# Optimization experiments

Measured on AMD Instinct MI355X. Metric: run time of the kernel, lower is better.

## Reference

```python
import jax, jax.numpy as jnp
import numpy as np

B, D, T = 16, 512, 2048
K, C = 8, 1024          # num_codebooks, codebook_size
CH = D // K             # chunk_size = 64
COMMIT = 0.25
EPS = 1e-8


def setup_inputs() -> dict:
    key = jax.random.key(0)
    k1, k2 = jax.random.split(key)
    x = jax.random.normal(k1, (B, D, T), dtype=jnp.float32)
    # kaiming-uniform-ish init for codebooks [K, C, CH]
    bound = float(np.sqrt(6.0 / CH))
    codebooks = jax.random.uniform(k2, (K, C, CH), dtype=jnp.float32,
                                   minval=-bound, maxval=bound)
    return {"x": x, "codebooks": codebooks}


def reference(x, codebooks):
    b, d, t = x.shape
    xc = x.reshape(b, K, CH, t)                       # [B,K,CH,T]
    x_norm = jnp.sum(xc * xc, axis=2)[:, :, None, :]  # [B,K,1,T]
    c_norm = jnp.sum(codebooks * codebooks, axis=2)[None, :, :, None]  # [1,K,C,1]
    cross = -2.0 * jnp.einsum('bkdt,kcd->bkct', xc, codebooks)         # [B,K,C,T]
    distances = x_norm + c_norm + cross
    indices = jnp.argmin(distances, axis=2)           # [B,K,T] int
    # gather nearest codewords -> [B,K,T,CH] -> [B,K,CH,T]
    q = codebooks[jnp.arange(K)[None, :, None], indices]
    q = jnp.transpose(q, (0, 1, 3, 2))                # [B,K,CH,T]
    # per-codebook usage histogram
    kk = jnp.broadcast_to(jnp.arange(K)[None, :, None], indices.shape)
    counts = jnp.zeros((K, C), dtype=jnp.float32).at[kk.ravel(), indices.ravel()].add(1.0)
    avg_probs = counts / (b * t)
    perplexity = jnp.exp(jnp.sum(-avg_probs * jnp.log(avg_probs + EPS), axis=1))
    # commitment losses
    sg = jax.lax.stop_gradient
    codebook_loss = jnp.mean((sg(xc) - q) ** 2)
    encoder_loss = jnp.mean((xc - sg(q)) ** 2)
    commit_loss = codebook_loss + COMMIT * encoder_loss
    # straight-through estimator
    quantized = xc + sg(q - xc)
    return quantized.reshape(b, d, t), commit_loss, perplexity
```

## Files before the change

kernel.cpp:

```cpp
#include <hip/hip_runtime.h>
#include <hip/hip_bf16.h>
#include <math.h>

#define B_   16
#define D_   512
#define T_   2048
#define K_   8
#define C_   1024
#define CH_  64
#define NEL_ (B_ * D_ * T_)
#define QOFF 16777216

#define WS_HCN   0
#define WS_CNT   32768
#define WS_SSE   65536
#define WS_CBS   66048

typedef __attribute__((ext_vector_type(8))) short   short8;
typedef __attribute__((ext_vector_type(8))) __bf16  bf16x8;
typedef __attribute__((ext_vector_type(4))) float   f32x4;

__device__ __forceinline__ unsigned short f2bf_rne(float f) {
    unsigned u = __builtin_bit_cast(unsigned, f);
    u = u + 0x7FFFu + ((u >> 16) & 1u);
    return (unsigned short)(u >> 16);
}

__device__ __forceinline__ void gload_lds16(const void* gsrc, void* ldst) {
    __builtin_amdgcn_global_load_lds(
        (const __attribute__((address_space(1))) unsigned int*)gsrc,
        (__attribute__((address_space(3))) unsigned int*)ldst,
        16, 0, 0);
}

__global__ void vq_prep(const float* __restrict__ cb,
                        unsigned char* __restrict__ cbS,
                        float* __restrict__ hcn) {
    int g   = blockIdx.x * 256 + threadIdx.x;
    int row = g >> 3;
    int s8  = g & 7;
    const float* src = cb + (size_t)row * CH_;

    short8 val;
#pragma unroll
    for (int j = 0; j < 8; ++j)
        val[j] = (short)f2bf_rne(-src[s8 * 8 + j]);
    *(short8*)(cbS + (size_t)row * 128 + ((s8 ^ (row & 7)) * 16)) = val;

    if (s8 == 0) {
        float s = 0.f;
#pragma unroll 8
        for (int ch = 0; ch < CH_; ++ch) {
            float v = src[ch];
            s = fmaf(v, v, s);
        }
        hcn[row] = 0.5f * s;
    }
}

#define LDSBUF 16384

__global__ __launch_bounds__(256, 4) void vq_main(
    const float* __restrict__ x,
    const float* __restrict__ cb,
    const unsigned char* __restrict__ cbS,
    const float* __restrict__ hcn,
    float* __restrict__ out,
    int* __restrict__ counts,
    double* __restrict__ sse)
{
    __shared__ __align__(16) unsigned char lds[2 * LDSBUF + 4096];
    float* hcnS = (float*)(lds + 2 * LDSBUF);

    const int tid  = threadIdx.x;
    const int lane = tid & 63;
    const int wave = tid >> 6;
    const int ln   = lane & 15;
    const int q    = lane >> 4;
    const int q4   = q * 4;

    const int bid = blockIdx.x;
    const int tc  = bid & 7;
    const int k   = (bid >> 3) & 7;
    const int b   = bid >> 6;
    const int t0  = tc * 256 + wave * 64;

    short8 bh[4][2];
    float  xn[4];
#pragma unroll
    for (int tt = 0; tt < 4; ++tt) {
        int t = t0 + tt * 16 + ln;
        float pn = 0.f;
#pragma unroll
        for (int ks = 0; ks < 2; ++ks) {
            const float* xp = x + ((size_t)(b * D_ + k * CH_ + ks * 32 + q * 8)) * T_ + t;
            short8 sh;
#pragma unroll
            for (int j = 0; j < 8; ++j) {
                float v = xp[(size_t)j * T_];
                pn = fmaf(v, v, pn);
                sh[j] = (short)f2bf_rne(v);
            }
            bh[tt][ks] = sh;
        }
        pn += __shfl_xor(pn, 16);
        pn += __shfl_xor(pn, 32);
        xn[tt] = pn;
    }

    const unsigned char* cbS_k = cbS + (size_t)k * C_ * 128;
    const float*         hcn_k = hcn + k * C_;

    for (int i = tid; i < C_; i += 256) hcnS[i] = hcn_k[i];

    {
        const unsigned char* src = cbS_k + wave * 4096 + lane * 16;
        unsigned char* dst = lds + wave * 4096;
#pragma unroll
        for (int i = 0; i < 4; ++i)
            gload_lds16(src + i * 1024, dst + i * 1024);
    }

    float md[4][4];
    int   mj[4][4];
#pragma unroll
    for (int tt = 0; tt < 4; ++tt)
#pragma unroll
        for (int r = 0; r < 4; ++r) { md[tt][r] = INFINITY; mj[tt][r] = 0; }

    for (int chunk = 0; chunk < 8; ++chunk) {
        __syncthreads();

        if (chunk < 7) {
            const unsigned char* src =
                cbS_k + (size_t)(chunk + 1) * 16384 + wave * 4096 + lane * 16;
            unsigned char* dst = lds + ((chunk + 1) & 1) * LDSBUF + wave * 4096;
#pragma unroll
            for (int i = 0; i < 4; ++i)
                gload_lds16(src + i * 1024, dst + i * 1024);
        }

        const unsigned char* buf = lds + (chunk & 1) * LDSBUF;
#pragma unroll
        for (int sub = 0; sub < 8; ++sub) {
            const unsigned char* rowb = buf + (sub * 16 + ln) * 128;
            f32x4 h4 = *(const f32x4*)(hcnS + chunk * 128 + sub * 16 + q4);
            f32x4 a[4];
#pragma unroll
            for (int tt = 0; tt < 4; ++tt) a[tt] = h4;
#pragma unroll
            for (int ks = 0; ks < 2; ++ks) {
                int cidx = ((ks * 4 + q) ^ (ln & 7)) * 16;
                bf16x8 ah = __builtin_bit_cast(bf16x8, *(const short8*)(rowb + cidx));
#pragma unroll
                for (int tt = 0; tt < 4; ++tt)
                    a[tt] = __builtin_amdgcn_mfma_f32_16x16x32_bf16(
                        ah, __builtin_bit_cast(bf16x8, bh[tt][ks]), a[tt], 0, 0, 0);
            }
            const int j = chunk * 8 + sub;
#pragma unroll
            for (int tt = 0; tt < 4; ++tt) {
#pragma unroll
                for (int r = 0; r < 4; ++r) {
                    bool lt = a[tt][r] < md[tt][r];
                    md[tt][r] = lt ? a[tt][r] : md[tt][r];
                    mj[tt][r] = lt ? j : mj[tt][r];
                }
            }
        }
    }

    double waveSse = 0.0;
    const float* cb_k = cb + (size_t)k * C_ * CH_;

#pragma unroll
    for (int tt = 0; tt < 4; ++tt) {
        const int t = t0 + tt * 16 + ln;

        float d1 = md[tt][0];
        int   c1 = mj[tt][0] * 16 + q4;
#pragma unroll
        for (int r = 1; r < 4; ++r) {
            float v  = md[tt][r];
            int   cv = mj[tt][r] * 16 + q4 + r;
            bool w = (v < d1) || (v == d1 && cv < c1);
            d1 = w ? v : d1;
            c1 = w ? cv : c1;
        }
#pragma unroll
        for (int off = 16; off <= 32; off <<= 1) {
            float ov = __shfl_xor(d1, off);
            int   oc = __shfl_xor(c1, off);
            bool w = (ov < d1) || (ov == d1 && oc < c1);
            d1 = w ? ov : d1;
            c1 = w ? oc : c1;
        }
        const int idx = c1;

        if (q == 0) {
            waveSse += (double)(xn[tt] + 2.0f * d1);
            atomicAdd(&counts[k * C_ + idx], 1);
        }

        const float* qrow = cb_k + (size_t)idx * CH_ + q * 16;
        float* op = out + ((size_t)(b * D_ + k * CH_ + q * 16)) * T_ + t;
#pragma unroll
        for (int jj = 0; jj < 4; ++jj) {
            float4 qv = *(const float4*)(qrow + 4 * jj);
            op[(size_t)(4 * jj + 0) * T_] = qv.x;
            op[(size_t)(4 * jj + 1) * T_] = qv.y;
            op[(size_t)(4 * jj + 2) * T_] = qv.z;
            op[(size_t)(4 * jj + 3) * T_] = qv.w;
        }
    }

    for (int off = 32; off > 0; off >>= 1) waveSse += __shfl_down(waveSse, off);
    if (lane == 0) atomicAdd(sse, waveSse);
}

__global__ void vq_final(const int* __restrict__ counts,
                         const double* __restrict__ sse,
                         float* __restrict__ out) {
    __shared__ double part[4];
    const int tid = threadIdx.x;
    const int k   = blockIdx.x;
    double local = 0.0;
    for (int j = tid; j < C_; j += 256) {
        double p = (double)counts[k * C_ + j] * (1.0 / (double)(B_ * T_));
        local += -p * log(p + 1e-8);
    }
    for (int off = 32; off > 0; off >>= 1) local += __shfl_down(local, off);
    if ((tid & 63) == 0) part[tid >> 6] = local;
    __syncthreads();
    if (tid == 0) {
        double sum = part[0] + part[1] + part[2] + part[3];
        out[QOFF + 1 + k] = (float)exp(sum);
        if (k == 0)
            out[QOFF] = (float)(1.25 * (*sse) / (double)NEL_);
    }
}

extern "C" void kernel_launch(void* const* d_in, const int* in_sizes, int n_in,
                              void* d_out, int out_size, void* d_ws, size_t ws_size,
                              hipStream_t stream) {
    const float* x  = (const float*)d_in[0];
    const float* cb = (const float*)d_in[1];
    float* out = (float*)d_out;

    float*         hcn    = (float*)((char*)d_ws + WS_HCN);
    int*           counts = (int*)((char*)d_ws + WS_CNT);
    double*        sse    = (double*)((char*)d_ws + WS_SSE);
    unsigned char* cbS    = (unsigned char*)((char*)d_ws + WS_CBS);

    hipMemsetAsync((char*)d_ws + WS_CNT, 0, 33024, stream);

    vq_prep<<<(K_ * C_ * 8) / 256, 256, 0, stream>>>(cb, cbS, hcn);
    vq_main<<<B_ * K_ * (T_ / 256), 256, 0, stream>>>(x, cb, cbS, hcn,
                                                      out, counts, sse);
    vq_final<<<K_, 256, 0, stream>>>(counts, sse, out);
}
```

Measured before the change: 222.3 us.

## Use 512-thread blocks, stage indices in LDS for coalesced output, fold memset into prep

Doubles the block size to 8 waves, each handling 32 time steps instead of 64, which halves per-wave MFMA accumulators and raises occupancy. Winning indices are staged in LDS so the output writeback becomes float4 stores contiguous along T instead of scattered scalar stores. The counters and SSE are zeroed inside the prep kernel, removing the separate memset launch. The trade-off is that each codebook tile read from LDS is reused across fewer time columns, and an extra block-wide barrier is added before writeback.

```diff
diff --git a/kernel.cpp b/kernel.cpp
--- a/kernel.cpp
+++ b/kernel.cpp
@@ -19,6 +19,7 @@
 typedef __attribute__((ext_vector_type(8))) short   short8;
 typedef __attribute__((ext_vector_type(8))) __bf16  bf16x8;
 typedef __attribute__((ext_vector_type(4))) float   f32x4;
+typedef __attribute__((ext_vector_type(4))) int     i32x4;
 
 __device__ __forceinline__ unsigned short f2bf_rne(float f) {
     unsigned u = __builtin_bit_cast(unsigned, f);
@@ -35,8 +36,13 @@
 
 __global__ void vq_prep(const float* __restrict__ cb,
                         unsigned char* __restrict__ cbS,
-                        float* __restrict__ hcn) {
+                        float* __restrict__ hcn,
+                        int* __restrict__ counts,
+                        double* __restrict__ sse) {
     int g   = blockIdx.x * 256 + threadIdx.x;
+    if (g < K_ * C_) counts[g] = 0;
+    if (g == 0) *sse = 0.0;
+
     int row = g >> 3;
     int s8  = g & 7;
     const float* src = cb + (size_t)row * CH_;
@@ -60,7 +66,7 @@
 
 #define LDSBUF 16384
 
-__global__ __launch_bounds__(256, 4) void vq_main(
+__global__ __launch_bounds__(512, 8) void vq_main(
     const float* __restrict__ x,
     const float* __restrict__ cb,
     const unsigned char* __restrict__ cbS,
@@ -69,8 +75,9 @@
     int* __restrict__ counts,
     double* __restrict__ sse)
 {
-    __shared__ __align__(16) unsigned char lds[2 * LDSBUF + 4096];
+    __shared__ __align__(16) unsigned char lds[2 * LDSBUF + 4096 + 1024];
     float* hcnS = (float*)(lds + 2 * LDSBUF);
+    int*   idxS = (int*)(lds + 2 * LDSBUF + 4096);
 
     const int tid  = threadIdx.x;
     const int lane = tid & 63;
@@ -83,13 +90,14 @@
     const int tc  = bid & 7;
     const int k   = (bid >> 3) & 7;
     const int b   = bid >> 6;
-    const int t0  = tc * 256 + wave * 64;
-
-    short8 bh[4][2];
-    float  xn[4];
-#pragma unroll
-    for (int tt = 0; tt < 4; ++tt) {
-        int t = t0 + tt * 16 + ln;
+    const int t0  = tc * 256;
+    const int tw  = t0 + wave * 32;
+
+    short8 bh[2][2];
+    float  xn[2];
+#pragma unroll
+    for (int tt = 0; tt < 2; ++tt) {
+        int t = tw + tt * 16 + ln;
         float pn = 0.f;
 #pragma unroll
         for (int ks = 0; ks < 2; ++ks) {
@@ -111,20 +119,20 @@
     const unsigned char* cbS_k = cbS + (size_t)k * C_ * 128;
     const float*         hcn_k = hcn + k * C_;
 
-    for (int i = tid; i < C_; i += 256) hcnS[i] = hcn_k[i];
+    for (int i = tid; i < C_; i += 512) hcnS[i] = hcn_k[i];
 
     {
-        const unsigned char* src = cbS_k + wave * 4096 + lane * 16;
-        unsigned char* dst = lds + wave * 4096;
-#pragma unroll
-        for (int i = 0; i < 4; ++i)
+        const unsigned char* src = cbS_k + wave * 2048 + lane * 16;
+        unsigned char* dst = lds + wave * 2048;
+#pragma unroll
+        for (int i = 0; i < 2; ++i)
             gload_lds16(src + i * 1024, dst + i * 1024);
     }
 
-    float md[4][4];
-    int   mj[4][4];
-#pragma unroll
-    for (int tt = 0; tt < 4; ++tt)
+    float md[2][4];
+    int   mj[2][4];
+#pragma unroll
+    for (int tt = 0; tt < 2; ++tt)
 #pragma unroll
         for (int r = 0; r < 4; ++r) { md[tt][r] = INFINITY; mj[tt][r] = 0; }
 
@@ -133,10 +141,10 @@
 
         if (chunk < 7) {
             const unsigned char* src =
-                cbS_k + (size_t)(chunk + 1) * 16384 + wave * 4096 + lane * 16;
-            unsigned char* dst = lds + ((chunk + 1) & 1) * LDSBUF + wave * 4096;
-#pragma unroll
-            for (int i = 0; i < 4; ++i)
+                cbS_k + (size_t)(chunk + 1) * 16384 + wave * 2048 + lane * 16;
+            unsigned char* dst = lds + ((chunk + 1) & 1) * LDSBUF + wave * 2048;
+#pragma unroll
+            for (int i = 0; i < 2; ++i)
                 gload_lds16(src + i * 1024, dst + i * 1024);
         }
 
@@ -145,21 +153,21 @@
         for (int sub = 0; sub < 8; ++sub) {
             const unsigned char* rowb = buf + (sub * 16 + ln) * 128;
             f32x4 h4 = *(const f32x4*)(hcnS + chunk * 128 + sub * 16 + q4);
-            f32x4 a[4];
-#pragma unroll
-            for (int tt = 0; tt < 4; ++tt) a[tt] = h4;
+            f32x4 a[2];
+            a[0] = h4;
+            a[1] = h4;
 #pragma unroll
             for (int ks = 0; ks < 2; ++ks) {
                 int cidx = ((ks * 4 + q) ^ (ln & 7)) * 16;
                 bf16x8 ah = __builtin_bit_cast(bf16x8, *(const short8*)(rowb + cidx));
 #pragma unroll
-                for (int tt = 0; tt < 4; ++tt)
+                for (int tt = 0; tt < 2; ++tt)
                     a[tt] = __builtin_amdgcn_mfma_f32_16x16x32_bf16(
                         ah, __builtin_bit_cast(bf16x8, bh[tt][ks]), a[tt], 0, 0, 0);
             }
             const int j = chunk * 8 + sub;
 #pragma unroll
-            for (int tt = 0; tt < 4; ++tt) {
+            for (int tt = 0; tt < 2; ++tt) {
 #pragma unroll
                 for (int r = 0; r < 4; ++r) {
                     bool lt = a[tt][r] < md[tt][r];
@@ -171,12 +179,9 @@
     }
 
     double waveSse = 0.0;
-    const float* cb_k = cb + (size_t)k * C_ * CH_;
-
-#pragma unroll
-    for (int tt = 0; tt < 4; ++tt) {
-        const int t = t0 + tt * 16 + ln;
-
+
+#pragma unroll
+    for (int tt = 0; tt < 2; ++tt) {
         float d1 = md[tt][0];
         int   c1 = mj[tt][0] * 16 + q4;
 #pragma unroll
@@ -195,27 +200,40 @@
             d1 = w ? ov : d1;
             c1 = w ? oc : c1;
         }
-        const int idx = c1;
 
         if (q == 0) {
             waveSse += (double)(xn[tt] + 2.0f * d1);
-            atomicAdd(&counts[k * C_ + idx], 1);
-        }
-
-        const float* qrow = cb_k + (size_t)idx * CH_ + q * 16;
-        float* op = out + ((size_t)(b * D_ + k * CH_ + q * 16)) * T_ + t;
-#pragma unroll
-        for (int jj = 0; jj < 4; ++jj) {
-            float4 qv = *(const float4*)(qrow + 4 * jj);
-            op[(size_t)(4 * jj + 0) * T_] = qv.x;
-            op[(size_t)(4 * jj + 1) * T_] = qv.y;
-            op[(size_t)(4 * jj + 2) * T_] = qv.z;
-            op[(size_t)(4 * jj + 3) * T_] = qv.w;
+            atomicAdd(&counts[k * C_ + c1], 1);
+            idxS[wave * 32 + tt * 16 + ln] = c1;
         }
     }
 
     for (int off = 32; off > 0; off >>= 1) waveSse += __shfl_down(waveSse, off);
     if (lane == 0) atomicAdd(sse, waveSse);
+
+    __syncthreads();
+
+    const float* cb_k = cb + (size_t)k * C_ * CH_;
+    i32x4 idx4 = *(const i32x4*)(idxS + 4 * lane);
+
+    float vals[4][8];
+#pragma unroll
+    for (int m = 0; m < 4; ++m) {
+        const float* rp = cb_k + (size_t)idx4[m] * CH_ + wave * 8;
+        f32x4 a0 = *(const f32x4*)rp;
+        f32x4 a1 = *(const f32x4*)(rp + 4);
+#pragma unroll
+        for (int jj = 0; jj < 4; ++jj) {
+            vals[m][jj]     = a0[jj];
+            vals[m][jj + 4] = a1[jj];
+        }
+    }
+#pragma unroll
+    for (int rr = 0; rr < 8; ++rr) {
+        f32x4 v = { vals[0][rr], vals[1][rr], vals[2][rr], vals[3][rr] };
+        *(f32x4*)(out + ((size_t)(b * D_ + k * CH_ + wave * 8 + rr)) * T_
+                      + t0 + 4 * lane) = v;
+    }
 }
 
 __global__ void vq_final(const int* __restrict__ counts,
@@ -252,10 +270,8 @@
     double*        sse    = (double*)((char*)d_ws + WS_SSE);
     unsigned char* cbS    = (unsigned char*)((char*)d_ws + WS_CBS);
 
-    hipMemsetAsync((char*)d_ws + WS_CNT, 0, 33024, stream);
-
-    vq_prep<<<(K_ * C_ * 8) / 256, 256, 0, stream>>>(cb, cbS, hcn);
-    vq_main<<<B_ * K_ * (T_ / 256), 256, 0, stream>>>(x, cb, cbS, hcn,
+    vq_prep<<<(K_ * C_ * 8) / 256, 256, 0, stream>>>(cb, cbS, hcn, counts, sse);
+    vq_main<<<B_ * K_ * (T_ / 256), 512, 0, stream>>>(x, cb, cbS, hcn,
                                                       out, counts, sse);
     vq_final<<<K_, 256, 0, stream>>>(counts, sse, out);
 }
```

New measurement: 247.4 us. 11.3% more time.

## Stage argmin indices in LDS and write output with coalesced float4 stores

Applied to the files above, without the earlier changes.

The output gather is restructured so each block stages its chosen codeword indices in shared memory, then each thread writes four consecutive time steps per channel as a float4 store instead of scattered scalar stores strided by T. Argmin slot indices are packed into one 32-bit register per tile to cut register pressure. The separate memset is folded into the prep kernel, and launch bounds drop from 4 to 2 waves per SIMD hint. Costs are an extra block barrier and a small LDS buffer, and the looser launch bounds may change occupancy.

```diff
diff --git a/kernel.cpp b/kernel.cpp
--- a/kernel.cpp
+++ b/kernel.cpp
@@ -19,6 +19,7 @@
 typedef __attribute__((ext_vector_type(8))) short   short8;
 typedef __attribute__((ext_vector_type(8))) __bf16  bf16x8;
 typedef __attribute__((ext_vector_type(4))) float   f32x4;
+typedef __attribute__((ext_vector_type(4))) int     i32x4;
 
 __device__ __forceinline__ unsigned short f2bf_rne(float f) {
     unsigned u = __builtin_bit_cast(unsigned, f);
@@ -35,8 +36,13 @@
 
 __global__ void vq_prep(const float* __restrict__ cb,
                         unsigned char* __restrict__ cbS,
-                        float* __restrict__ hcn) {
+                        float* __restrict__ hcn,
+                        int* __restrict__ counts,
+                        double* __restrict__ sse) {
     int g   = blockIdx.x * 256 + threadIdx.x;
+    if (g < K_ * C_) counts[g] = 0;
+    if (g == 0) *sse = 0.0;
+
     int row = g >> 3;
     int s8  = g & 7;
     const float* src = cb + (size_t)row * CH_;
@@ -60,7 +66,7 @@
 
 #define LDSBUF 16384
 
-__global__ __launch_bounds__(256, 4) void vq_main(
+__global__ __launch_bounds__(256, 2) void vq_main(
     const float* __restrict__ x,
     const float* __restrict__ cb,
     const unsigned char* __restrict__ cbS,
@@ -69,8 +75,9 @@
     int* __restrict__ counts,
     double* __restrict__ sse)
 {
-    __shared__ __align__(16) unsigned char lds[2 * LDSBUF + 4096];
+    __shared__ __align__(16) unsigned char lds[2 * LDSBUF + 4096 + 1024];
     float* hcnS = (float*)(lds + 2 * LDSBUF);
+    int*   idxS = (int*)(lds + 2 * LDSBUF + 4096);
 
     const int tid  = threadIdx.x;
     const int lane = tid & 63;
@@ -83,13 +90,14 @@
     const int tc  = bid & 7;
     const int k   = (bid >> 3) & 7;
     const int b   = bid >> 6;
-    const int t0  = tc * 256 + wave * 64;
+    const int t0b = tc * 256;
+    const int tw  = t0b + wave * 64;
 
     short8 bh[4][2];
     float  xn[4];
 #pragma unroll
     for (int tt = 0; tt < 4; ++tt) {
-        int t = t0 + tt * 16 + ln;
+        int t = tw + tt * 16 + ln;
         float pn = 0.f;
 #pragma unroll
         for (int ks = 0; ks < 2; ++ks) {
@@ -121,12 +129,14 @@
             gload_lds16(src + i * 1024, dst + i * 1024);
     }
 
-    float md[4][4];
-    int   mj[4][4];
-#pragma unroll
-    for (int tt = 0; tt < 4; ++tt)
-#pragma unroll
-        for (int r = 0; r < 4; ++r) { md[tt][r] = INFINITY; mj[tt][r] = 0; }
+    float    md[4][4];
+    unsigned mjp[4];
+#pragma unroll
+    for (int tt = 0; tt < 4; ++tt) {
+        mjp[tt] = 0u;
+#pragma unroll
+        for (int r = 0; r < 4; ++r) md[tt][r] = INFINITY;
+    }
 
     for (int chunk = 0; chunk < 8; ++chunk) {
         __syncthreads();
@@ -157,32 +167,30 @@
                     a[tt] = __builtin_amdgcn_mfma_f32_16x16x32_bf16(
                         ah, __builtin_bit_cast(bf16x8, bh[tt][ks]), a[tt], 0, 0, 0);
             }
-            const int j = chunk * 8 + sub;
+            const unsigned j = (unsigned)(chunk * 8 + sub);
 #pragma unroll
             for (int tt = 0; tt < 4; ++tt) {
 #pragma unroll
                 for (int r = 0; r < 4; ++r) {
                     bool lt = a[tt][r] < md[tt][r];
                     md[tt][r] = lt ? a[tt][r] : md[tt][r];
-                    mj[tt][r] = lt ? j : mj[tt][r];
+                    unsigned upd = (mjp[tt] & ~(0xFFu << (8 * r))) | (j << (8 * r));
+                    mjp[tt] = lt ? upd : mjp[tt];
                 }
             }
         }
     }
 
     double waveSse = 0.0;
-    const float* cb_k = cb + (size_t)k * C_ * CH_;
 
 #pragma unroll
     for (int tt = 0; tt < 4; ++tt) {
-        const int t = t0 + tt * 16 + ln;
-
         float d1 = md[tt][0];
-        int   c1 = mj[tt][0] * 16 + q4;
+        int   c1 = (int)(mjp[tt] & 0xFFu) * 16 + q4;
 #pragma unroll
         for (int r = 1; r < 4; ++r) {
             float v  = md[tt][r];
-            int   cv = mj[tt][r] * 16 + q4 + r;
+            int   cv = (int)((mjp[tt] >> (8 * r)) & 0xFFu) * 16 + q4 + r;
             bool w = (v < d1) || (v == d1 && cv < c1);
             d1 = w ? v : d1;
             c1 = w ? cv : c1;
@@ -195,27 +203,35 @@
             d1 = w ? ov : d1;
             c1 = w ? oc : c1;
         }
-        const int idx = c1;
 
         if (q == 0) {
             waveSse += (double)(xn[tt] + 2.0f * d1);
-            atomicAdd(&counts[k * C_ + idx], 1);
-        }
-
-        const float* qrow = cb_k + (size_t)idx * CH_ + q * 16;
-        float* op = out + ((size_t)(b * D_ + k * CH_ + q * 16)) * T_ + t;
-#pragma unroll
-        for (int jj = 0; jj < 4; ++jj) {
-            float4 qv = *(const float4*)(qrow + 4 * jj);
-            op[(size_t)(4 * jj + 0) * T_] = qv.x;
-            op[(size_t)(4 * jj + 1) * T_] = qv.y;
-            op[(size_t)(4 * jj + 2) * T_] = qv.z;
-            op[(size_t)(4 * jj + 3) * T_] = qv.w;
+            atomicAdd(&counts[k * C_ + c1], 1);
+            idxS[wave * 64 + tt * 16 + ln] = c1;
         }
     }
 
     for (int off = 32; off > 0; off >>= 1) waveSse += __shfl_down(waveSse, off);
     if (lane == 0) atomicAdd(sse, waveSse);
+
+    __syncthreads();
+
+    const float* cb_k = cb + (size_t)k * C_ * CH_;
+    i32x4 idx4 = *(const i32x4*)(idxS + 4 * lane);
+#pragma unroll
+    for (int h = 0; h < 4; ++h) {
+        f32x4 g[4];
+#pragma unroll
+        for (int m = 0; m < 4; ++m)
+            g[m] = *(const f32x4*)(cb_k + (size_t)idx4[m] * CH_
+                                   + wave * 16 + h * 4);
+#pragma unroll
+        for (int rr = 0; rr < 4; ++rr) {
+            f32x4 v = { g[0][rr], g[1][rr], g[2][rr], g[3][rr] };
+            *(f32x4*)(out + ((size_t)(b * D_ + k * CH_ + wave * 16 + h * 4
+                                      + rr)) * T_ + t0b + 4 * lane) = v;
+        }
+    }
 }
 
 __global__ void vq_final(const int* __restrict__ counts,
@@ -252,9 +268,7 @@
     double*        sse    = (double*)((char*)d_ws + WS_SSE);
     unsigned char* cbS    = (unsigned char*)((char*)d_ws + WS_CBS);
 
-    hipMemsetAsync((char*)d_ws + WS_CNT, 0, 33024, stream);
-
-    vq_prep<<<(K_ * C_ * 8) / 256, 256, 0, stream>>>(cb, cbS, hcn);
+    vq_prep<<<(K_ * C_ * 8) / 256, 256, 0, stream>>>(cb, cbS, hcn, counts, sse);
     vq_main<<<B_ * K_ * (T_ / 256), 256, 0, stream>>>(x, cb, cbS, hcn,
                                                       out, counts, sse);
     vq_final<<<K_, 256, 0, stream>>>(counts, sse, out);
```

Result: faster. 204.4 us (-8.0%).
